# Kernel tuning notes

Measured on AMD Instinct MI355X. Metric: run time of the kernel, lower is better.

## Reference

```python
import jax, jax.numpy as jnp
import numpy as np

NUM_NODES = 40000
NUM_EDGES = 400000
DIM = 128
NUM_REL = 502  # num_relation * 2
NUM_HEAD = 1


def setup_inputs() -> dict:
    key = jax.random.key(0)
    ks = jax.random.split(key, 16)
    d = DIM
    return {
        "curr_stat": jax.random.normal(ks[0], (NUM_NODES, d), jnp.float32),
        "last_stat": jax.random.normal(ks[1], (NUM_NODES, d), jnp.float32),
        "relemb_weight": jax.random.normal(ks[2], (NUM_REL, d), jnp.float32),
        "selfrel_weight": jax.random.normal(ks[3], (1, d), jnp.float32),
        "Wq": jax.random.normal(ks[4], (2 * d, d), jnp.float32) * (1.0 / np.sqrt(2 * d)),
        "bq": jax.random.normal(ks[5], (d,), jnp.float32) * 0.02,
        "Wk": jax.random.normal(ks[6], (2 * d, d), jnp.float32) * (1.0 / np.sqrt(2 * d)),
        "bk": jax.random.normal(ks[7], (d,), jnp.float32) * 0.02,
        "Wv": jax.random.normal(ks[8], (d, d), jnp.float32) * (1.0 / np.sqrt(d)),
        "bv": jax.random.normal(ks[9], (d,), jnp.float32) * 0.02,
        "dyn_weight": jax.random.normal(ks[10], (d, d), jnp.float32) * (1.0 / np.sqrt(d)),
        "edge_index": jax.random.randint(ks[11], (2, NUM_EDGES), 0, NUM_NODES, jnp.int32),
        "edge_type": jax.random.randint(ks[12], (NUM_EDGES,), 0, NUM_REL, jnp.int32),
    }


def _segment_softmax(scores, seg, num_segments):
    # scores: [E, H]; softmax over edges sharing the same destination segment
    m = jax.ops.segment_max(scores, seg, num_segments=num_segments)  # [N, H]
    e = jnp.exp(scores - m[seg])
    s = jax.ops.segment_sum(e, seg, num_segments=num_segments)  # [N, H]
    return e / s[seg]


def reference(curr_stat, last_stat, relemb_weight, selfrel_weight,
              Wq, bq, Wk, bk, Wv, bv, dyn_weight,
              edge_index, edge_type):
    N, D = curr_stat.shape
    H = NUM_HEAD
    HD = D // H

    # append self-loop edges for every node, with the dedicated self-relation
    loop = jnp.arange(N, dtype=edge_index.dtype)
    src = jnp.concatenate([edge_index[0], loop])  # [E_total]
    dst = jnp.concatenate([edge_index[1], loop])  # [E_total]
    type_emb = jnp.concatenate(
        [relemb_weight[edge_type], jnp.broadcast_to(selfrel_weight, (N, D))], axis=0)

    E = src.shape[0]
    # linear projections (x @ W + b); torch Linear stores W transposed, same math
    q = (jnp.concatenate([curr_stat[dst], type_emb], -1) @ Wq + bq).reshape(E, H, HD)
    k = (jnp.concatenate([last_stat[src], type_emb], -1) @ Wk + bk).reshape(E, H, HD)
    v = (last_stat[src] @ Wv + bv).reshape(E, H, HD)

    attn = jnp.sum(q * k, axis=-1) / np.sqrt(HD).astype(np.float32)  # [E, H]

    dyn_prob = _segment_softmax(attn, dst, N)   # [E, H]
    sta_prob = _segment_softmax(-attn, dst, N)  # [E, H]

    counts = jax.ops.segment_sum(jnp.ones((E,), jnp.float32), dst, num_segments=N)
    denom = jnp.maximum(counts, 1.0)[:, None]  # scatter-mean denominator

    feat_dyn = jax.ops.segment_sum((dyn_prob[..., None] * v).reshape(E, D), dst,
                                   num_segments=N) / denom
    feat_sta = jax.ops.segment_sum((sta_prob[..., None] * v).reshape(E, D), dst,
                                   num_segments=N) / denom

    # stack (feat_sta, feat_dyn @ dyn_weight) -> [2, N, D]
    return jnp.stack([feat_sta, feat_dyn @ dyn_weight])
```

## Files before the change

kernel.cpp:

```cpp
#include <hip/hip_runtime.h>
#include <hip/hip_bf16.h>
#include <math.h>

#define DIMC 128

typedef __attribute__((ext_vector_type(8))) short short8;
typedef __attribute__((ext_vector_type(4))) float floatx4;

static __device__ __forceinline__ unsigned pk2(float lo, float hi) {
    __hip_bfloat162 h = __float22bfloat162_rn(make_float2(lo, hi));
    return *(unsigned*)&h;
}
static __device__ __forceinline__ unsigned short f2bf(float x) {
    union { float f; unsigned int u; } v; v.f = x;
    unsigned int r = v.u + 0x7FFFu + ((v.u >> 16) & 1u);
    return (unsigned short)(r >> 16);
}
static __device__ __forceinline__ float2 bf2f2(unsigned int u) {
    union { unsigned int i; float f; } a, b;
    a.i = u << 16; b.i = u & 0xFFFF0000u;
    return make_float2(a.f, b.f);
}

struct PrepArgs { const float* W[4]; unsigned short* F[4]; };

__global__ __launch_bounds__(64) void prep_wfrag(PrepArgs a)
{
    int mat = blockIdx.y;
    int ts  = blockIdx.x;
    int s = ts & 3, t = ts >> 2;
    int lane = threadIdx.x;
    int q = lane >> 4, c = lane & 15;
    const float* W = a.W[mat];
    unsigned short o[8];
    #pragma unroll
    for (int j = 0; j < 8; ++j)
        o[j] = f2bf(W[(long)(s * 32 + q * 8 + j) * DIMC + t * 16 + c]);
    uint4 u;
    u.x = (unsigned)o[0] | ((unsigned)o[1] << 16);
    u.y = (unsigned)o[2] | ((unsigned)o[3] << 16);
    u.z = (unsigned)o[4] | ((unsigned)o[5] << 16);
    u.w = (unsigned)o[6] | ((unsigned)o[7] << 16);
    ((uint4*)a.F[mat])[ts * 64 + lane] = u;
}

struct GemmM3 {
    const float*          Af[3];
    const unsigned short* Ab[3];
    const unsigned short* F[3];
    const float*          bias[3];
    float*                outf[3];
    unsigned short*       outb[3];
    int                   ostride[3];
    int                   ooff[3];
};

__global__ __launch_bounds__(256) void gemm_mfma(GemmM3 g, int M)
{
    const int which = blockIdx.y;
    const float*          __restrict__ Af   = g.Af[which];
    const unsigned short* __restrict__ Ab   = g.Ab[which];
    const unsigned short* __restrict__ F    = g.F[which];
    const float*          __restrict__ bias = g.bias[which];
    float*          __restrict__ outf = g.outf[which];
    unsigned short* __restrict__ outb = g.outb[which];
    const int ostride = g.ostride[which];
    const int ooff    = g.ooff[which];

    const int wave = threadIdx.x >> 6;
    const int lane = threadIdx.x & 63;
    const int q = lane >> 4, c = lane & 15;
    const int rowbase = blockIdx.x * 64 + wave * 16;

    short8 wf[8][4];
    const uint4* Fp = (const uint4*)F;
    #pragma unroll
    for (int t = 0; t < 8; ++t)
        #pragma unroll
        for (int s = 0; s < 4; ++s) {
            uint4 u = Fp[(t * 4 + s) * 64 + lane];
            wf[t][s] = *(short8*)&u;
        }

    floatx4 acc[8];
    #pragma unroll
    for (int t = 0; t < 8; ++t) {
        float b = bias ? bias[t * 16 + c] : 0.0f;
        acc[t] = (floatx4){b, b, b, b};
    }

    short8 af[4];
    if (Af) {
        const float* Ar = Af + (long)(rowbase + c) * DIMC + q * 8;
        #pragma unroll
        for (int s = 0; s < 4; ++s) {
            float4 x0 = *(const float4*)(Ar + s * 32);
            float4 x1 = *(const float4*)(Ar + s * 32 + 4);
            uint4 u;
            u.x = pk2(x0.x, x0.y);
            u.y = pk2(x0.z, x0.w);
            u.z = pk2(x1.x, x1.y);
            u.w = pk2(x1.z, x1.w);
            af[s] = *(short8*)&u;
        }
    } else {
        const unsigned short* Ar = Ab + (long)(rowbase + c) * DIMC + q * 8;
        #pragma unroll
        for (int s = 0; s < 4; ++s) {
            uint4 u = *(const uint4*)(Ar + s * 32);
            af[s] = *(short8*)&u;
        }
    }

    #pragma unroll
    for (int t = 0; t < 8; ++t)
        #pragma unroll
        for (int s = 0; s < 4; ++s)
            acc[t] = __builtin_amdgcn_mfma_f32_16x16x32_bf16(af[s], wf[t][s], acc[t], 0, 0, 0);

    if (outf) {
        #pragma unroll
        for (int t = 0; t < 8; ++t)
            #pragma unroll
            for (int r = 0; r < 4; ++r)
                outf[(long)(rowbase + q * 4 + r) * DIMC + t * 16 + c] = acc[t][r];
    } else {
        #pragma unroll
        for (int t = 0; t < 8; ++t)
            #pragma unroll
            for (int r = 0; r < 4; ++r) {
                float other = __shfl_xor(acc[t][r], 1);
                if ((lane & 1) == 0) {
                    unsigned word = pk2(acc[t][r], other);
                    ((unsigned*)outb)[((long)(rowbase + q * 4 + r) * 64 + t * 8 + (c >> 1))
                                      * (long)ostride + ooff] = word;
                }
            }
    }
}

__global__ __launch_bounds__(128) void rel_proj(
    const float* __restrict__ relemb, const float* __restrict__ selfrel,
    const float* __restrict__ Wq, const float* __restrict__ bq,
    const float* __restrict__ Wk, const float* __restrict__ bk,
    uint2* __restrict__ QKre, int R)
{
    int t = blockIdx.x;
    int c = threadIdx.x;
    const float* row = (t < R) ? (relemb + (long)t * DIMC) : selfrel;
    float aq = bq[c], ak = bk[c];
    for (int k = 0; k < DIMC; ++k) {
        float a = row[k];
        aq = fmaf(a, Wq[(long)(DIMC + k) * DIMC + c], aq);
        ak = fmaf(a, Wk[(long)(DIMC + k) * DIMC + c], ak);
    }
    float aqo = __shfl_xor(aq, 1);
    float ako = __shfl_xor(ak, 1);
    if ((c & 1) == 0)
        QKre[(long)t * 64 + (c >> 1)] = make_uint2(pk2(aq, aqo), pk2(ak, ako));
}

__global__ void zero_int(int* __restrict__ p, int n) {
    int i = blockIdx.x * blockDim.x + threadIdx.x;
    if (i < n) p[i] = 0;
}

__global__ void hist_kernel(const int* __restrict__ dst, int* __restrict__ deg, int E) {
    int e = blockIdx.x * blockDim.x + threadIdx.x;
    if (e < E) atomicAdd(&deg[dst[e]], 1);
}

__global__ __launch_bounds__(256) void partial_sums(const int* __restrict__ deg,
                                                    int* __restrict__ partial, int N)
{
    __shared__ int sh[256];
    int t = threadIdx.x;
    int beg = blockIdx.x * 1024 + t * 4;
    int s = 0;
    if (beg + 3 < N) { int4 v = *(const int4*)(deg + beg); s = v.x + v.y + v.z + v.w; }
    else { for (int j = 0; j < 4; ++j) if (beg + j < N) s += deg[beg + j]; }
    sh[t] = s;
    __syncthreads();
    for (int d = 128; d >= 1; d >>= 1) {
        if (t < d) sh[t] += sh[t + d];
        __syncthreads();
    }
    if (t == 0) partial[blockIdx.x] = sh[0];
}

__global__ __launch_bounds__(256) void scan_partials(int* __restrict__ partial, int nb)
{
    __shared__ int sh[256];
    int t = threadIdx.x;
    sh[t] = (t < nb) ? partial[t] : 0;
    __syncthreads();
    for (int d = 1; d < 256; d <<= 1) {
        int v = (t >= d) ? sh[t - d] : 0;
        __syncthreads();
        sh[t] += v;
        __syncthreads();
    }
    if (t < nb) partial[t] = (t == 0) ? 0 : sh[t - 1];
}

__global__ __launch_bounds__(256) void write_offsets(const int* __restrict__ deg,
                                                     const int* __restrict__ partial,
                                                     int* __restrict__ offs,
                                                     int* __restrict__ cursor, int N)
{
    __shared__ int sh[256];
    int t = threadIdx.x;
    int beg = blockIdx.x * 1024 + t * 4;
    int d0 = 0, d1 = 0, d2 = 0, d3 = 0;
    if (beg + 3 < N) { int4 v = *(const int4*)(deg + beg); d0 = v.x; d1 = v.y; d2 = v.z; d3 = v.w; }
    else {
        if (beg < N)     d0 = deg[beg];
        if (beg + 1 < N) d1 = deg[beg + 1];
        if (beg + 2 < N) d2 = deg[beg + 2];
        if (beg + 3 < N) d3 = deg[beg + 3];
    }
    int s = d0 + d1 + d2 + d3;
    sh[t] = s;
    __syncthreads();
    for (int d = 1; d < 256; d <<= 1) {
        int v = (t >= d) ? sh[t - d] : 0;
        __syncthreads();
        sh[t] += v;
        __syncthreads();
    }
    int base = partial[blockIdx.x] + sh[t] - s;
    int o0 = base, o1 = o0 + d0, o2 = o1 + d1, o3 = o2 + d2;
    if (beg < N)     { offs[beg]     = o0; cursor[beg]     = o0; }
    if (beg + 1 < N) { offs[beg + 1] = o1; cursor[beg + 1] = o1; }
    if (beg + 2 < N) { offs[beg + 2] = o2; cursor[beg + 2] = o2; }
    if (beg + 3 < N) { offs[beg + 3] = o3; cursor[beg + 3] = o3; }
}

__global__ void scatter_kernel(const int* __restrict__ src, const int* __restrict__ dst,
                               const int* __restrict__ etype, int* __restrict__ cursor,
                               int2* __restrict__ sedge, int E)
{
    int e = blockIdx.x * blockDim.x + threadIdx.x;
    if (e < E) {
        int d = dst[e];
        int p = atomicAdd(&cursor[d], 1);
        sedge[p] = make_int2(src[e], etype[e]);
    }
}

__global__ __launch_bounds__(256) void node_kernel(
    const float* __restrict__ Qn,
    const uint2* __restrict__ KV,
    const uint2* __restrict__ QKre,
    const int* __restrict__ offs, const int* __restrict__ deg,
    const int2* __restrict__ sedge,
    float* __restrict__ out_sta, unsigned* __restrict__ feat_dyn,
    int N, int R)
{
    int n = (blockIdx.x * blockDim.x + threadIdx.x) >> 6;
    int lane = threadIdx.x & 63;
    if (n >= N) return;

    const float cs = 0.08838834764831845f * 1.4426950408889634f;
    int base = offs[n];
    int dcnt = deg[n];

    float2 qn = ((const float2*)(Qn + (long)n * DIMC))[lane];

    uint2 kvs = KV[(unsigned)n * 64u + lane];
    uint2 qks = QKre[(unsigned)R * 64u + lane];
    float2 ks = bf2f2(kvs.x), vs = bf2f2(kvs.y);
    float2 qr = bf2f2(qks.x), kr = bf2f2(qks.y);
    float p = (qn.x + qr.x) * (ks.x + kr.x) + (qn.y + qr.y) * (ks.y + kr.y);
    #pragma unroll
    for (int m = 32; m >= 1; m >>= 1) p += __shfl_xor(p, m);
    float a_self = p * cs;

    float m_dyn = a_self, s_dyn = 1.0f;
    float m_sta = -a_self, s_sta = 1.0f;
    float2 accd = vs;
    float2 accs = vs;

    int i = 0;
    for (; i + 4 <= dcnt; i += 4) {
        int2 e0 = sedge[base + i],     e1 = sedge[base + i + 1];
        int2 e2 = sedge[base + i + 2], e3 = sedge[base + i + 3];

        uint2 kv0 = KV[(unsigned)e0.x * 64u + lane];
        uint2 kv1 = KV[(unsigned)e1.x * 64u + lane];
        uint2 kv2 = KV[(unsigned)e2.x * 64u + lane];
        uint2 kv3 = KV[(unsigned)e3.x * 64u + lane];
        uint2 t0 = QKre[(unsigned)e0.y * 64u + lane];
        uint2 t1 = QKre[(unsigned)e1.y * 64u + lane];
        uint2 t2 = QKre[(unsigned)e2.y * 64u + lane];
        uint2 t3 = QKre[(unsigned)e3.y * 64u + lane];

        float2 kn0 = bf2f2(kv0.x), v0 = bf2f2(kv0.y);
        float2 kn1 = bf2f2(kv1.x), v1 = bf2f2(kv1.y);
        float2 kn2 = bf2f2(kv2.x), v2 = bf2f2(kv2.y);
        float2 kn3 = bf2f2(kv3.x), v3 = bf2f2(kv3.y);
        float2 q0 = bf2f2(t0.x), k0 = bf2f2(t0.y);
        float2 q1 = bf2f2(t1.x), k1 = bf2f2(t1.y);
        float2 q2 = bf2f2(t2.x), k2 = bf2f2(t2.y);
        float2 q3 = bf2f2(t3.x), k3 = bf2f2(t3.y);

        float p0 = (qn.x + q0.x) * (kn0.x + k0.x) + (qn.y + q0.y) * (kn0.y + k0.y);
        float p1 = (qn.x + q1.x) * (kn1.x + k1.x) + (qn.y + q1.y) * (kn1.y + k1.y);
        float p2 = (qn.x + q2.x) * (kn2.x + k2.x) + (qn.y + q2.y) * (kn2.y + k2.y);
        float p3 = (qn.x + q3.x) * (kn3.x + k3.x) + (qn.y + q3.y) * (kn3.y + k3.y);
        #pragma unroll
        for (int m = 32; m >= 1; m >>= 1) {
            p0 += __shfl_xor(p0, m);
            p1 += __shfl_xor(p1, m);
            p2 += __shfl_xor(p2, m);
            p3 += __shfl_xor(p3, m);
        }
        float a0 = p0 * cs, a1 = p1 * cs, a2 = p2 * cs, a3 = p3 * cs;

        float mx = fmaxf(fmaxf(a0, a1), fmaxf(a2, a3));
        float mn = fmaxf(m_dyn, mx);
        float f  = exp2f(m_dyn - mn);
        float w0 = exp2f(a0 - mn), w1 = exp2f(a1 - mn);
        float w2 = exp2f(a2 - mn), w3 = exp2f(a3 - mn);
        s_dyn = fmaf(s_dyn, f, (w0 + w1) + (w2 + w3));
        accd.x = fmaf(accd.x, f, fmaf(w0, v0.x, fmaf(w1, v1.x, fmaf(w2, v2.x, w3 * v3.x))));
        accd.y = fmaf(accd.y, f, fmaf(w0, v0.y, fmaf(w1, v1.y, fmaf(w2, v2.y, w3 * v3.y))));
        m_dyn = mn;

        float nmx = -fminf(fminf(a0, a1), fminf(a2, a3));
        float ms = fmaxf(m_sta, nmx);
        float fs = exp2f(m_sta - ms);
        float u0 = exp2f(-a0 - ms), u1 = exp2f(-a1 - ms);
        float u2 = exp2f(-a2 - ms), u3 = exp2f(-a3 - ms);
        s_sta = fmaf(s_sta, fs, (u0 + u1) + (u2 + u3));
        accs.x = fmaf(accs.x, fs, fmaf(u0, v0.x, fmaf(u1, v1.x, fmaf(u2, v2.x, u3 * v3.x))));
        accs.y = fmaf(accs.y, fs, fmaf(u0, v0.y, fmaf(u1, v1.y, fmaf(u2, v2.y, u3 * v3.y))));
        m_sta = ms;
    }

    for (; i < dcnt; ++i) {
        int2 e = sedge[base + i];
        uint2 kv = KV[(unsigned)e.x * 64u + lane];
        uint2 tt = QKre[(unsigned)e.y * 64u + lane];
        float2 kn = bf2f2(kv.x), v = bf2f2(kv.y);
        float2 q2 = bf2f2(tt.x), k2 = bf2f2(tt.y);
        float pp = (qn.x + q2.x) * (kn.x + k2.x) + (qn.y + q2.y) * (kn.y + k2.y);
        #pragma unroll
        for (int m = 32; m >= 1; m >>= 1) pp += __shfl_xor(pp, m);
        float a = pp * cs;

        float mn = fmaxf(m_dyn, a);
        float fd = exp2f(m_dyn - mn);
        float wd = exp2f(a - mn);
        s_dyn = fmaf(s_dyn, fd, wd);
        accd.x = fmaf(accd.x, fd, wd * v.x);
        accd.y = fmaf(accd.y, fd, wd * v.y);
        m_dyn = mn;

        float ms = fmaxf(m_sta, -a);
        float fs = exp2f(m_sta - ms);
        float ws_ = exp2f(-a - ms);
        s_sta = fmaf(s_sta, fs, ws_);
        accs.x = fmaf(accs.x, fs, ws_ * v.x);
        accs.y = fmaf(accs.y, fs, ws_ * v.y);
        m_sta = ms;
    }

    float denom = (float)(dcnt + 1);
    float id_ = 1.0f / (s_dyn * denom);
    float is_ = 1.0f / (s_sta * denom);
    ((float2*)(out_sta + (long)n * DIMC))[lane] = make_float2(accs.x * is_, accs.y * is_);
    feat_dyn[(unsigned)n * 64u + lane] = pk2(accd.x * id_, accd.y * id_);
}

extern "C" void kernel_launch(void* const* d_in, const int* in_sizes, int n_in,
                              void* d_out, int out_size, void* d_ws, size_t ws_size,
                              hipStream_t stream)
{
    const float* curr    = (const float*)d_in[0];
    const float* last    = (const float*)d_in[1];
    const float* relemb  = (const float*)d_in[2];
    const float* selfrel = (const float*)d_in[3];
    const float* Wq      = (const float*)d_in[4];
    const float* bq      = (const float*)d_in[5];
    const float* Wk      = (const float*)d_in[6];
    const float* bk      = (const float*)d_in[7];
    const float* Wv      = (const float*)d_in[8];
    const float* bv      = (const float*)d_in[9];
    const float* dynw    = (const float*)d_in[10];
    const int*   eidx    = (const int*)d_in[11];
    const int*   etype   = (const int*)d_in[12];
    float* out = (float*)d_out;

    const int N = in_sizes[0] / DIMC;
    const int E = in_sizes[12];
    const int R = in_sizes[2] / DIMC;
    const int* esrc = eidx;
    const int* edst = eidx + E;

    char* wp = (char*)d_ws;
    auto alloc = [&](size_t bytes) { char* r = wp; wp += (bytes + 15) & ~(size_t)15; return r; };
    size_t nd = (size_t)N * DIMC;
    float*          Qn    = (float*)alloc(nd * 4);
    uint2*          KV    = (uint2*)alloc((size_t)N * 64 * 8);
    unsigned short* Fdb   = (unsigned short*)alloc(nd * 2);
    uint2*          QKre  = (uint2*)alloc((size_t)(R + 1) * 64 * 8);
    unsigned short* FWq   = (unsigned short*)alloc(2048 * 8 * 2);
    unsigned short* FWk   = (unsigned short*)alloc(2048 * 8 * 2);
    unsigned short* FWv   = (unsigned short*)alloc(2048 * 8 * 2);
    unsigned short* FWd   = (unsigned short*)alloc(2048 * 8 * 2);
    int*            deg   = (int*)alloc((size_t)N * 4);
    int*            offs  = (int*)alloc((size_t)N * 4);
    int*            cursor= (int*)alloc((size_t)N * 4);
    int2*           sedge = (int2*)alloc((size_t)E * 8);
    int*            partial = (int*)alloc(256 * 4);

    const int gblk = N / 64;
    const int sblk = (N + 1023) / 1024;

    PrepArgs pa;
    pa.W[0] = Wq;   pa.F[0] = FWq;
    pa.W[1] = Wk;   pa.F[1] = FWk;
    pa.W[2] = Wv;   pa.F[2] = FWv;
    pa.W[3] = dynw; pa.F[3] = FWd;
    hipLaunchKernelGGL(prep_wfrag, dim3(32, 4), dim3(64), 0, stream, pa);

    GemmM3 qkv;
    qkv.Af[0] = curr; qkv.Ab[0] = nullptr; qkv.F[0] = FWq; qkv.bias[0] = nullptr;
    qkv.outf[0] = Qn; qkv.outb[0] = nullptr; qkv.ostride[0] = 1; qkv.ooff[0] = 0;
    qkv.Af[1] = last; qkv.Ab[1] = nullptr; qkv.F[1] = FWk; qkv.bias[1] = nullptr;
    qkv.outf[1] = nullptr; qkv.outb[1] = (unsigned short*)KV; qkv.ostride[1] = 2; qkv.ooff[1] = 0;
    qkv.Af[2] = last; qkv.Ab[2] = nullptr; qkv.F[2] = FWv; qkv.bias[2] = bv;
    qkv.outf[2] = nullptr; qkv.outb[2] = (unsigned short*)KV; qkv.ostride[2] = 2; qkv.ooff[2] = 1;
    hipLaunchKernelGGL(gemm_mfma, dim3(gblk, 3), dim3(256), 0, stream, qkv, N);

    hipLaunchKernelGGL(rel_proj, dim3(R + 1), dim3(128), 0, stream,
                       relemb, selfrel, Wq, bq, Wk, bk, QKre, R);
    hipLaunchKernelGGL(zero_int, dim3((N + 255) / 256), dim3(256), 0, stream, deg, N);
    hipLaunchKernelGGL(hist_kernel, dim3((E + 255) / 256), dim3(256), 0, stream, edst, deg, E);
    hipLaunchKernelGGL(partial_sums, dim3(sblk), dim3(256), 0, stream, deg, partial, N);
    hipLaunchKernelGGL(scan_partials, dim3(1), dim3(256), 0, stream, partial, sblk);
    hipLaunchKernelGGL(write_offsets, dim3(sblk), dim3(256), 0, stream,
                       deg, partial, offs, cursor, N);
    hipLaunchKernelGGL(scatter_kernel, dim3((E + 255) / 256), dim3(256), 0, stream,
                       esrc, edst, etype, cursor, sedge, E);
    hipLaunchKernelGGL(node_kernel, dim3((N + 3) / 4), dim3(256), 0, stream,
                       Qn, KV, QKre, offs, deg, sedge, out, (unsigned*)Fdb, N, R);

    GemmM3 fin;
    fin.Af[0] = nullptr; fin.Ab[0] = Fdb; fin.F[0] = FWd; fin.bias[0] = nullptr;
    fin.outf[0] = out + nd; fin.outb[0] = nullptr; fin.ostride[0] = 1; fin.ooff[0] = 0;
    fin.Af[1] = nullptr; fin.Ab[1] = Fdb; fin.F[1] = FWd; fin.bias[1] = nullptr;
    fin.outf[1] = out + nd; fin.outb[1] = nullptr; fin.ostride[1] = 1; fin.ooff[1] = 0;
    fin.Af[2] = nullptr; fin.Ab[2] = Fdb; fin.F[2] = FWd; fin.bias[2] = nullptr;
    fin.outf[2] = out + nd; fin.outb[2] = nullptr; fin.ostride[2] = 1; fin.ooff[2] = 0;
    hipLaunchKernelGGL(gemm_mfma, dim3(gblk, 1), dim3(256), 0, stream, fin, N);
}
```

Baseline: 243.0 us.

## Split node edges across half-waves and merge prep, relation projection into MFMA GEMM

The node kernel now gives each destination node two 32-lane halves that each process alternate pairs of edges with 16-byte vector loads. The halves merge their online-softmax state with a cross-half shuffle at the end, which halves the shuffle-reduction depth per edge and widens the gathers. The scalar relation-projection kernel and the zero-fill kernel are removed. Relation embeddings are copied into a staging buffer and projected by the MFMA GEMM as two extra batched slices, and weight-fragment prep, the embedding copy and the degree zeroing share one launch. This cuts launch count and the slow FMA loop, at the cost of masked extra edge loads and added bounds checks in the GEMM.

```diff
diff --git a/kernel.cpp b/kernel.cpp
--- a/kernel.cpp
+++ b/kernel.cpp
@@ -22,42 +22,63 @@
     return make_float2(a.f, b.f);
 }
 
-struct PrepArgs { const float* W[4]; unsigned short* F[4]; };
-
-__global__ __launch_bounds__(64) void prep_wfrag(PrepArgs a)
-{
-    int mat = blockIdx.y;
-    int ts  = blockIdx.x;
-    int s = ts & 3, t = ts >> 2;
+struct PrepArgs {
+    const float* W[6];
+    unsigned short* F[6];
+    const float* relemb; const float* selfrel;
+    float* TypeEmb;
+    int* deg;
+    int R; int N;
+};
+
+__global__ __launch_bounds__(64) void prep_all(PrepArgs a)
+{
+    int b = blockIdx.x;
     int lane = threadIdx.x;
-    int q = lane >> 4, c = lane & 15;
-    const float* W = a.W[mat];
-    unsigned short o[8];
-    #pragma unroll
-    for (int j = 0; j < 8; ++j)
-        o[j] = f2bf(W[(long)(s * 32 + q * 8 + j) * DIMC + t * 16 + c]);
-    uint4 u;
-    u.x = (unsigned)o[0] | ((unsigned)o[1] << 16);
-    u.y = (unsigned)o[2] | ((unsigned)o[3] << 16);
-    u.z = (unsigned)o[4] | ((unsigned)o[5] << 16);
-    u.w = (unsigned)o[6] | ((unsigned)o[7] << 16);
-    ((uint4*)a.F[mat])[ts * 64 + lane] = u;
-}
-
-struct GemmM3 {
-    const float*          Af[3];
-    const unsigned short* Ab[3];
-    const unsigned short* F[3];
-    const float*          bias[3];
-    float*                outf[3];
-    unsigned short*       outb[3];
-    int                   ostride[3];
-    int                   ooff[3];
+    if (b < 192) {
+        int mat = b >> 5, ts = b & 31;
+        int s = ts & 3, t = ts >> 2;
+        int q = lane >> 4, c = lane & 15;
+        const float* W = a.W[mat];
+        unsigned short o[8];
+        #pragma unroll
+        for (int j = 0; j < 8; ++j)
+            o[j] = f2bf(W[(long)(s * 32 + q * 8 + j) * DIMC + t * 16 + c]);
+        uint4 u;
+        u.x = (unsigned)o[0] | ((unsigned)o[1] << 16);
+        u.y = (unsigned)o[2] | ((unsigned)o[3] << 16);
+        u.z = (unsigned)o[4] | ((unsigned)o[5] << 16);
+        u.w = (unsigned)o[6] | ((unsigned)o[7] << 16);
+        ((uint4*)a.F[mat])[ts * 64 + lane] = u;
+    } else if (b < 192 + a.R + 1) {
+        int r = b - 192;
+        const float* src = (r < a.R) ? (a.relemb + (long)r * DIMC) : a.selfrel;
+        float2 v = ((const float2*)src)[lane];
+        ((float2*)(a.TypeEmb + (long)r * DIMC))[lane] = v;
+    } else {
+        int i = (b - (192 + a.R + 1)) * 64 + lane;
+        if (i < a.N) a.deg[i] = 0;
+    }
+}
+
+struct GemmM5 {
+    const float*          Af[5];
+    const unsigned short* Ab[5];
+    const unsigned short* F[5];
+    const float*          bias[5];
+    float*                outf[5];
+    unsigned short*       outb[5];
+    int                   ostride[5];
+    int                   ooff[5];
+    int                   M[5];
 };
 
-__global__ __launch_bounds__(256) void gemm_mfma(GemmM3 g, int M)
+__global__ __launch_bounds__(256) void gemm_mfma(GemmM5 g)
 {
     const int which = blockIdx.y;
+    const int M = g.M[which];
+    if (blockIdx.x * 64 >= M) return;
+
     const float*          __restrict__ Af   = g.Af[which];
     const unsigned short* __restrict__ Ab   = g.Ab[which];
     const unsigned short* __restrict__ F    = g.F[which];
@@ -89,9 +110,10 @@
         acc[t] = (floatx4){b, b, b, b};
     }
 
+    int rowA = rowbase + c; if (rowA > M - 1) rowA = M - 1;
     short8 af[4];
     if (Af) {
-        const float* Ar = Af + (long)(rowbase + c) * DIMC + q * 8;
+        const float* Ar = Af + (long)rowA * DIMC + q * 8;
         #pragma unroll
         for (int s = 0; s < 4; ++s) {
             float4 x0 = *(const float4*)(Ar + s * 32);
@@ -104,7 +126,7 @@
             af[s] = *(short8*)&u;
         }
     } else {
-        const unsigned short* Ar = Ab + (long)(rowbase + c) * DIMC + q * 8;
+        const unsigned short* Ar = Ab + (long)rowA * DIMC + q * 8;
         #pragma unroll
         for (int s = 0; s < 4; ++s) {
             uint4 u = *(const uint4*)(Ar + s * 32);
@@ -122,47 +144,25 @@
         #pragma unroll
         for (int t = 0; t < 8; ++t)
             #pragma unroll
-            for (int r = 0; r < 4; ++r)
-                outf[(long)(rowbase + q * 4 + r) * DIMC + t * 16 + c] = acc[t][r];
+            for (int r = 0; r < 4; ++r) {
+                int row = rowbase + q * 4 + r;
+                if (row < M)
+                    outf[(long)row * DIMC + t * 16 + c] = acc[t][r];
+            }
     } else {
         #pragma unroll
         for (int t = 0; t < 8; ++t)
             #pragma unroll
             for (int r = 0; r < 4; ++r) {
                 float other = __shfl_xor(acc[t][r], 1);
-                if ((lane & 1) == 0) {
+                int row = rowbase + q * 4 + r;
+                if ((lane & 1) == 0 && row < M) {
                     unsigned word = pk2(acc[t][r], other);
-                    ((unsigned*)outb)[((long)(rowbase + q * 4 + r) * 64 + t * 8 + (c >> 1))
+                    ((unsigned*)outb)[((long)row * 64 + t * 8 + (c >> 1))
                                       * (long)ostride + ooff] = word;
                 }
             }
     }
-}
-
-__global__ __launch_bounds__(128) void rel_proj(
-    const float* __restrict__ relemb, const float* __restrict__ selfrel,
-    const float* __restrict__ Wq, const float* __restrict__ bq,
-    const float* __restrict__ Wk, const float* __restrict__ bk,
-    uint2* __restrict__ QKre, int R)
-{
-    int t = blockIdx.x;
-    int c = threadIdx.x;
-    const float* row = (t < R) ? (relemb + (long)t * DIMC) : selfrel;
-    float aq = bq[c], ak = bk[c];
-    for (int k = 0; k < DIMC; ++k) {
-        float a = row[k];
-        aq = fmaf(a, Wq[(long)(DIMC + k) * DIMC + c], aq);
-        ak = fmaf(a, Wk[(long)(DIMC + k) * DIMC + c], ak);
-    }
-    float aqo = __shfl_xor(aq, 1);
-    float ako = __shfl_xor(ak, 1);
-    if ((c & 1) == 0)
-        QKre[(long)t * 64 + (c >> 1)] = make_uint2(pk2(aq, aqo), pk2(ak, ako));
-}
-
-__global__ void zero_int(int* __restrict__ p, int n) {
-    int i = blockIdx.x * blockDim.x + threadIdx.x;
-    if (i < n) p[i] = 0;
 }
 
 __global__ void hist_kernel(const int* __restrict__ dst, int* __restrict__ deg, int E) {
@@ -250,127 +250,154 @@
 
 __global__ __launch_bounds__(256) void node_kernel(
     const float* __restrict__ Qn,
-    const uint2* __restrict__ KV,
-    const uint2* __restrict__ QKre,
+    const uint4* __restrict__ KV4,
+    const uint4* __restrict__ QK4,
     const int* __restrict__ offs, const int* __restrict__ deg,
     const int2* __restrict__ sedge,
-    float* __restrict__ out_sta, unsigned* __restrict__ feat_dyn,
+    float* __restrict__ out_sta, uint2* __restrict__ feat_dyn,
     int N, int R)
 {
     int n = (blockIdx.x * blockDim.x + threadIdx.x) >> 6;
     int lane = threadIdx.x & 63;
     if (n >= N) return;
+    const int hl = lane & 31;
+    const int h  = lane >> 5;
 
     const float cs = 0.08838834764831845f * 1.4426950408889634f;
     int base = offs[n];
     int dcnt = deg[n];
 
-    float2 qn = ((const float2*)(Qn + (long)n * DIMC))[lane];
-
-    uint2 kvs = KV[(unsigned)n * 64u + lane];
-    uint2 qks = QKre[(unsigned)R * 64u + lane];
-    float2 ks = bf2f2(kvs.x), vs = bf2f2(kvs.y);
-    float2 qr = bf2f2(qks.x), kr = bf2f2(qks.y);
-    float p = (qn.x + qr.x) * (ks.x + kr.x) + (qn.y + qr.y) * (ks.y + kr.y);
-    #pragma unroll
-    for (int m = 32; m >= 1; m >>= 1) p += __shfl_xor(p, m);
-    float a_self = p * cs;
-
-    float m_dyn = a_self, s_dyn = 1.0f;
-    float m_sta = -a_self, s_sta = 1.0f;
-    float2 accd = vs;
-    float2 accs = vs;
-
-    int i = 0;
-    for (; i + 4 <= dcnt; i += 4) {
-        int2 e0 = sedge[base + i],     e1 = sedge[base + i + 1];
-        int2 e2 = sedge[base + i + 2], e3 = sedge[base + i + 3];
-
-        uint2 kv0 = KV[(unsigned)e0.x * 64u + lane];
-        uint2 kv1 = KV[(unsigned)e1.x * 64u + lane];
-        uint2 kv2 = KV[(unsigned)e2.x * 64u + lane];
-        uint2 kv3 = KV[(unsigned)e3.x * 64u + lane];
-        uint2 t0 = QKre[(unsigned)e0.y * 64u + lane];
-        uint2 t1 = QKre[(unsigned)e1.y * 64u + lane];
-        uint2 t2 = QKre[(unsigned)e2.y * 64u + lane];
-        uint2 t3 = QKre[(unsigned)e3.y * 64u + lane];
-
-        float2 kn0 = bf2f2(kv0.x), v0 = bf2f2(kv0.y);
-        float2 kn1 = bf2f2(kv1.x), v1 = bf2f2(kv1.y);
-        float2 kn2 = bf2f2(kv2.x), v2 = bf2f2(kv2.y);
-        float2 kn3 = bf2f2(kv3.x), v3 = bf2f2(kv3.y);
-        float2 q0 = bf2f2(t0.x), k0 = bf2f2(t0.y);
-        float2 q1 = bf2f2(t1.x), k1 = bf2f2(t1.y);
-        float2 q2 = bf2f2(t2.x), k2 = bf2f2(t2.y);
-        float2 q3 = bf2f2(t3.x), k3 = bf2f2(t3.y);
-
-        float p0 = (qn.x + q0.x) * (kn0.x + k0.x) + (qn.y + q0.y) * (kn0.y + k0.y);
-        float p1 = (qn.x + q1.x) * (kn1.x + k1.x) + (qn.y + q1.y) * (kn1.y + k1.y);
-        float p2 = (qn.x + q2.x) * (kn2.x + k2.x) + (qn.y + q2.y) * (kn2.y + k2.y);
-        float p3 = (qn.x + q3.x) * (kn3.x + k3.x) + (qn.y + q3.y) * (kn3.y + k3.y);
-        #pragma unroll
-        for (int m = 32; m >= 1; m >>= 1) {
-            p0 += __shfl_xor(p0, m);
-            p1 += __shfl_xor(p1, m);
-            p2 += __shfl_xor(p2, m);
-            p3 += __shfl_xor(p3, m);
-        }
-        float a0 = p0 * cs, a1 = p1 * cs, a2 = p2 * cs, a3 = p3 * cs;
-
-        float mx = fmaxf(fmaxf(a0, a1), fmaxf(a2, a3));
-        float mn = fmaxf(m_dyn, mx);
-        float f  = exp2f(m_dyn - mn);
-        float w0 = exp2f(a0 - mn), w1 = exp2f(a1 - mn);
-        float w2 = exp2f(a2 - mn), w3 = exp2f(a3 - mn);
-        s_dyn = fmaf(s_dyn, f, (w0 + w1) + (w2 + w3));
-        accd.x = fmaf(accd.x, f, fmaf(w0, v0.x, fmaf(w1, v1.x, fmaf(w2, v2.x, w3 * v3.x))));
-        accd.y = fmaf(accd.y, f, fmaf(w0, v0.y, fmaf(w1, v1.y, fmaf(w2, v2.y, w3 * v3.y))));
-        m_dyn = mn;
-
-        float nmx = -fminf(fminf(a0, a1), fminf(a2, a3));
-        float ms = fmaxf(m_sta, nmx);
-        float fs = exp2f(m_sta - ms);
-        float u0 = exp2f(-a0 - ms), u1 = exp2f(-a1 - ms);
-        float u2 = exp2f(-a2 - ms), u3 = exp2f(-a3 - ms);
-        s_sta = fmaf(s_sta, fs, (u0 + u1) + (u2 + u3));
-        accs.x = fmaf(accs.x, fs, fmaf(u0, v0.x, fmaf(u1, v1.x, fmaf(u2, v2.x, u3 * v3.x))));
-        accs.y = fmaf(accs.y, fs, fmaf(u0, v0.y, fmaf(u1, v1.y, fmaf(u2, v2.y, u3 * v3.y))));
-        m_sta = ms;
-    }
-
-    for (; i < dcnt; ++i) {
-        int2 e = sedge[base + i];
-        uint2 kv = KV[(unsigned)e.x * 64u + lane];
-        uint2 tt = QKre[(unsigned)e.y * 64u + lane];
-        float2 kn = bf2f2(kv.x), v = bf2f2(kv.y);
-        float2 q2 = bf2f2(tt.x), k2 = bf2f2(tt.y);
-        float pp = (qn.x + q2.x) * (kn.x + k2.x) + (qn.y + q2.y) * (kn.y + k2.y);
-        #pragma unroll
-        for (int m = 32; m >= 1; m >>= 1) pp += __shfl_xor(pp, m);
-        float a = pp * cs;
-
-        float mn = fmaxf(m_dyn, a);
-        float fd = exp2f(m_dyn - mn);
-        float wd = exp2f(a - mn);
-        s_dyn = fmaf(s_dyn, fd, wd);
-        accd.x = fmaf(accd.x, fd, wd * v.x);
-        accd.y = fmaf(accd.y, fd, wd * v.y);
-        m_dyn = mn;
-
-        float ms = fmaxf(m_sta, -a);
-        float fs = exp2f(m_sta - ms);
-        float ws_ = exp2f(-a - ms);
-        s_sta = fmaf(s_sta, fs, ws_);
-        accs.x = fmaf(accs.x, fs, ws_ * v.x);
-        accs.y = fmaf(accs.y, fs, ws_ * v.y);
-        m_sta = ms;
-    }
-
-    float denom = (float)(dcnt + 1);
-    float id_ = 1.0f / (s_dyn * denom);
-    float is_ = 1.0f / (s_sta * denom);
-    ((float2*)(out_sta + (long)n * DIMC))[lane] = make_float2(accs.x * is_, accs.y * is_);
-    feat_dyn[(unsigned)n * 64u + lane] = pk2(accd.x * id_, accd.y * id_);
+    float4 qn = ((const float4*)(Qn + (long)n * DIMC))[hl];
+
+    uint4 kvs = KV4[(unsigned)n * 32u + hl];
+    uint4 qks = QK4[(unsigned)R * 32u + hl];
+    {
+        float2 k0 = bf2f2(kvs.x), k1 = bf2f2(kvs.z);
+        float2 qr0 = bf2f2(qks.x), qr1 = bf2f2(qks.z);
+        float2 kr0 = bf2f2(qks.y), kr1 = bf2f2(qks.w);
+        float p = (qn.x + qr0.x) * (k0.x + kr0.x)
+                + (qn.y + qr0.y) * (k0.y + kr0.y)
+                + (qn.z + qr1.x) * (k1.x + kr1.x)
+                + (qn.w + qr1.y) * (k1.y + kr1.y);
+        #pragma unroll
+        for (int m = 16; m >= 1; m >>= 1) p += __shfl_xor(p, m);
+        kvs.x = __float_as_uint(p);
+        qks.x = 0;
+        float a_self = p * cs;
+        float2 v0 = bf2f2(kvs.y), v1 = bf2f2(kvs.w);
+        float m_d, s_d, m_s, s_s; float4 accd, accs;
+        if (h == 0) {
+            m_d = a_self;  s_d = 1.0f;
+            m_s = -a_self; s_s = 1.0f;
+            accd = make_float4(v0.x, v0.y, v1.x, v1.y);
+            accs = accd;
+        } else {
+            m_d = -1e30f; s_d = 0.0f;
+            m_s = -1e30f; s_s = 0.0f;
+            accd = make_float4(0.f, 0.f, 0.f, 0.f);
+            accs = accd;
+        }
+
+        int T = (dcnt + 3) >> 2;
+        for (int it = 0; it < T; ++it) {
+            int iA = 4 * it + 2 * h, iB = iA + 1;
+            bool vA = iA < dcnt, vB = iB < dcnt;
+            int2 eA = sedge[vA ? (base + iA) : 0];
+            int2 eB = sedge[vB ? (base + iB) : 0];
+            uint4 kvA = KV4[(unsigned)eA.x * 32u + hl];
+            uint4 kvB = KV4[(unsigned)eB.x * 32u + hl];
+            uint4 qkA = QK4[(unsigned)eA.y * 32u + hl];
+            uint4 qkB = QK4[(unsigned)eB.y * 32u + hl];
+
+            float2 ka0 = bf2f2(kvA.x), ka1 = bf2f2(kvA.z);
+            float2 qa0 = bf2f2(qkA.x), qa1 = bf2f2(qkA.z);
+            float2 ra0 = bf2f2(qkA.y), ra1 = bf2f2(qkA.w);
+            float pA = (qn.x + qa0.x) * (ka0.x + ra0.x)
+                     + (qn.y + qa0.y) * (ka0.y + ra0.y)
+                     + (qn.z + qa1.x) * (ka1.x + ra1.x)
+                     + (qn.w + qa1.y) * (ka1.y + ra1.y);
+            float2 kb0 = bf2f2(kvB.x), kb1 = bf2f2(kvB.z);
+            float2 qb0 = bf2f2(qkB.x), qb1 = bf2f2(qkB.z);
+            float2 rb0 = bf2f2(qkB.y), rb1 = bf2f2(qkB.w);
+            float pB = (qn.x + qb0.x) * (kb0.x + rb0.x)
+                     + (qn.y + qb0.y) * (kb0.y + rb0.y)
+                     + (qn.z + qb1.x) * (kb1.x + rb1.x)
+                     + (qn.w + qb1.y) * (kb1.y + rb1.y);
+            #pragma unroll
+            for (int m = 16; m >= 1; m >>= 1) {
+                pA += __shfl_xor(pA, m);
+                pB += __shfl_xor(pB, m);
+            }
+            float aA = pA * cs, aB = pB * cs;
+            float dA = vA ? aA : -1e30f, dB = vB ? aB : -1e30f;
+            float nA = vA ? -aA : -1e30f, nB = vB ? -aB : -1e30f;
+
+            float2 va0 = bf2f2(kvA.y), va1 = bf2f2(kvA.w);
+            float2 vb0 = bf2f2(kvB.y), vb1 = bf2f2(kvB.w);
+
+            {
+                float mn = fmaxf(m_d, fmaxf(dA, dB));
+                float f  = exp2f(m_d - mn);
+                float wA = vA ? exp2f(dA - mn) : 0.0f;
+                float wB = vB ? exp2f(dB - mn) : 0.0f;
+                s_d = fmaf(s_d, f, wA + wB);
+                accd.x = fmaf(accd.x, f, fmaf(wA, va0.x, wB * vb0.x));
+                accd.y = fmaf(accd.y, f, fmaf(wA, va0.y, wB * vb0.y));
+                accd.z = fmaf(accd.z, f, fmaf(wA, va1.x, wB * vb1.x));
+                accd.w = fmaf(accd.w, f, fmaf(wA, va1.y, wB * vb1.y));
+                m_d = mn;
+            }
+            {
+                float mn = fmaxf(m_s, fmaxf(nA, nB));
+                float f  = exp2f(m_s - mn);
+                float wA = vA ? exp2f(nA - mn) : 0.0f;
+                float wB = vB ? exp2f(nB - mn) : 0.0f;
+                s_s = fmaf(s_s, f, wA + wB);
+                accs.x = fmaf(accs.x, f, fmaf(wA, va0.x, wB * vb0.x));
+                accs.y = fmaf(accs.y, f, fmaf(wA, va0.y, wB * vb0.y));
+                accs.z = fmaf(accs.z, f, fmaf(wA, va1.x, wB * vb1.x));
+                accs.w = fmaf(accs.w, f, fmaf(wA, va1.y, wB * vb1.y));
+                m_s = mn;
+            }
+        }
+
+        {
+            float mo = __shfl_xor(m_d, 32), so = __shfl_xor(s_d, 32);
+            float4 ao;
+            ao.x = __shfl_xor(accd.x, 32); ao.y = __shfl_xor(accd.y, 32);
+            ao.z = __shfl_xor(accd.z, 32); ao.w = __shfl_xor(accd.w, 32);
+            float M = fmaxf(m_d, mo);
+            float f0 = exp2f(m_d - M), f1 = exp2f(mo - M);
+            s_d = fmaf(s_d, f0, so * f1);
+            accd.x = fmaf(accd.x, f0, ao.x * f1);
+            accd.y = fmaf(accd.y, f0, ao.y * f1);
+            accd.z = fmaf(accd.z, f0, ao.z * f1);
+            accd.w = fmaf(accd.w, f0, ao.w * f1);
+        }
+        {
+            float mo = __shfl_xor(m_s, 32), so = __shfl_xor(s_s, 32);
+            float4 ao;
+            ao.x = __shfl_xor(accs.x, 32); ao.y = __shfl_xor(accs.y, 32);
+            ao.z = __shfl_xor(accs.z, 32); ao.w = __shfl_xor(accs.w, 32);
+            float M = fmaxf(m_s, mo);
+            float f0 = exp2f(m_s - M), f1 = exp2f(mo - M);
+            s_s = fmaf(s_s, f0, so * f1);
+            accs.x = fmaf(accs.x, f0, ao.x * f1);
+            accs.y = fmaf(accs.y, f0, ao.y * f1);
+            accs.z = fmaf(accs.z, f0, ao.z * f1);
+            accs.w = fmaf(accs.w, f0, ao.w * f1);
+        }
+
+        if (h == 0) {
+            float denom = (float)(dcnt + 1);
+            float id_ = 1.0f / (s_d * denom);
+            float is_ = 1.0f / (s_s * denom);
+            ((float4*)(out_sta + (long)n * DIMC))[hl] =
+                make_float4(accs.x * is_, accs.y * is_, accs.z * is_, accs.w * is_);
+            feat_dyn[(unsigned)n * 32u + hl] =
+                make_uint2(pk2(accd.x * id_, accd.y * id_), pk2(accd.z * id_, accd.w * id_));
+        }
+    }
 }
 
 extern "C" void kernel_launch(void* const* d_in, const int* in_sizes, int n_in,
@@ -402,13 +429,12 @@
     auto alloc = [&](size_t bytes) { char* r = wp; wp += (bytes + 15) & ~(size_t)15; return r; };
     size_t nd = (size_t)N * DIMC;
     float*          Qn    = (float*)alloc(nd * 4);
-    uint2*          KV    = (uint2*)alloc((size_t)N * 64 * 8);
+    uint4*          KV    = (uint4*)alloc((size_t)N * 32 * 16);
     unsigned short* Fdb   = (unsigned short*)alloc(nd * 2);
-    uint2*          QKre  = (uint2*)alloc((size_t)(R + 1) * 64 * 8);
-    unsigned short* FWq   = (unsigned short*)alloc(2048 * 8 * 2);
-    unsigned short* FWk   = (unsigned short*)alloc(2048 * 8 * 2);
-    unsigned short* FWv   = (unsigned short*)alloc(2048 * 8 * 2);
-    unsigned short* FWd   = (unsigned short*)alloc(2048 * 8 * 2);
+    uint4*          QKre  = (uint4*)alloc((size_t)(R + 1) * 32 * 16);
+    float*          TypeEmb = (float*)alloc((size_t)(R + 2) * DIMC * 4);
+    unsigned short* FW[6];
+    for (int m = 0; m < 6; ++m) FW[m] = (unsigned short*)alloc(2048 * 8 * 2);
     int*            deg   = (int*)alloc((size_t)N * 4);
     int*            offs  = (int*)alloc((size_t)N * 4);
     int*            cursor= (int*)alloc((size_t)N * 4);
@@ -419,24 +445,14 @@
     const int sblk = (N + 1023) / 1024;
 
     PrepArgs pa;
-    pa.W[0] = Wq;   pa.F[0] = FWq;
-    pa.W[1] = Wk;   pa.F[1] = FWk;
-    pa.W[2] = Wv;   pa.F[2] = FWv;
-    pa.W[3] = dynw; pa.F[3] = FWd;
-    hipLaunchKernelGGL(prep_wfrag, dim3(32, 4), dim3(64), 0, stream, pa);
-
-    GemmM3 qkv;
-    qkv.Af[0] = curr; qkv.Ab[0] = nullptr; qkv.F[0] = FWq; qkv.bias[0] = nullptr;
-    qkv.outf[0] = Qn; qkv.outb[0] = nullptr; qkv.ostride[0] = 1; qkv.ooff[0] = 0;
-    qkv.Af[1] = last; qkv.Ab[1] = nullptr; qkv.F[1] = FWk; qkv.bias[1] = nullptr;
-    qkv.outf[1] = nullptr; qkv.outb[1] = (unsigned short*)KV; qkv.ostride[1] = 2; qkv.ooff[1] = 0;
-    qkv.Af[2] = last; qkv.Ab[2] = nullptr; qkv.F[2] = FWv; qkv.bias[2] = bv;
-    qkv.outf[2] = nullptr; qkv.outb[2] = (unsigned short*)KV; qkv.ostride[2] = 2; qkv.ooff[2] = 1;
-    hipLaunchKernelGGL(gemm_mfma, dim3(gblk, 3), dim3(256), 0, stream, qkv, N);
-
-    hipLaunchKernelGGL(rel_proj, dim3(R + 1), dim3(128), 0, stream,
-                       relemb, selfrel, Wq, bq, Wk, bk, QKre, R);
-    hipLaunchKernelGGL(zero_int, dim3((N + 255) / 256), dim3(256), 0, stream, deg, N);
+    pa.W[0] = Wq;   pa.W[1] = Wk;   pa.W[2] = Wv;
+    pa.W[3] = dynw; pa.W[4] = Wq + (size_t)DIMC * DIMC; pa.W[5] = Wk + (size_t)DIMC * DIMC;
+    for (int m = 0; m < 6; ++m) pa.F[m] = FW[m];
+    pa.relemb = relemb; pa.selfrel = selfrel; pa.TypeEmb = TypeEmb;
+    pa.deg = deg; pa.R = R; pa.N = N;
+    int pgrid = 192 + (R + 1) + (N + 63) / 64;
+    hipLaunchKernelGGL(prep_all, dim3(pgrid), dim3(64), 0, stream, pa);
+
     hipLaunchKernelGGL(hist_kernel, dim3((E + 255) / 256), dim3(256), 0, stream, edst, deg, E);
     hipLaunchKernelGGL(partial_sums, dim3(sblk), dim3(256), 0, stream, deg, partial, N);
     hipLaunchKernelGGL(scan_partials, dim3(1), dim3(256), 0, stream, partial, sblk);
@@ -444,15 +460,27 @@
                        deg, partial, offs, cursor, N);
     hipLaunchKernelGGL(scatter_kernel, dim3((E + 255) / 256), dim3(256), 0, stream,
                        esrc, edst, etype, cursor, sedge, E);
+
+    GemmM5 g5;
+    for (int s = 0; s < 5; ++s) { g5.Ab[s] = nullptr; g5.outf[s] = nullptr; g5.outb[s] = nullptr; }
+    g5.Af[0] = curr;    g5.F[0] = FW[0]; g5.bias[0] = nullptr; g5.outf[0] = Qn;
+    g5.ostride[0] = 1;  g5.ooff[0] = 0;  g5.M[0] = N;
+    g5.Af[1] = last;    g5.F[1] = FW[1]; g5.bias[1] = nullptr; g5.outb[1] = (unsigned short*)KV;
+    g5.ostride[1] = 2;  g5.ooff[1] = 0;  g5.M[1] = N;
+    g5.Af[2] = last;    g5.F[2] = FW[2]; g5.bias[2] = bv;      g5.outb[2] = (unsigned short*)KV;
+    g5.ostride[2] = 2;  g5.ooff[2] = 1;  g5.M[2] = N;
+    g5.Af[3] = TypeEmb; g5.F[3] = FW[4]; g5.bias[3] = bq;      g5.outb[3] = (unsigned short*)QKre;
+    g5.ostride[3] = 2;  g5.ooff[3] = 0;  g5.M[3] = R + 1;
+    g5.Af[4] = TypeEmb; g5.F[4] = FW[5]; g5.bias[4] = bk;      g5.outb[4] = (unsigned short*)QKre;
+    g5.ostride[4] = 2;  g5.ooff[4] = 1;  g5.M[4] = R + 1;
+    hipLaunchKernelGGL(gemm_mfma, dim3(gblk, 5), dim3(256), 0, stream, g5);
+
     hipLaunchKernelGGL(node_kernel, dim3((N + 3) / 4), dim3(256), 0, stream,
-                       Qn, KV, QKre, offs, deg, sedge, out, (unsigned*)Fdb, N, R);
-
-    GemmM3 fin;
-    fin.Af[0] = nullptr; fin.Ab[0] = Fdb; fin.F[0] = FWd; fin.bias[0] = nullptr;
-    fin.outf[0] = out + nd; fin.outb[0] = nullptr; fin.ostride[0] = 1; fin.ooff[0] = 0;
-    fin.Af[1] = nullptr; fin.Ab[1] = Fdb; fin.F[1] = FWd; fin.bias[1] = nullptr;
-    fin.outf[1] = out + nd; fin.outb[1] = nullptr; fin.ostride[1] = 1; fin.ooff[1] = 0;
-    fin.Af[2] = nullptr; fin.Ab[2] = Fdb; fin.F[2] = FWd; fin.bias[2] = nullptr;
-    fin.outf[2] = out + nd; fin.outb[2] = nullptr; fin.ostride[2] = 1; fin.ooff[2] = 0;
-    hipLaunchKernelGGL(gemm_mfma, dim3(gblk, 1), dim3(256), 0, stream, fin, N);
-}
+                       Qn, KV, QKre, offs, deg, sedge, out, (uint2*)Fdb, N, R);
+
+    GemmM5 gf;
+    for (int s = 0; s < 5; ++s) { gf.Af[s] = nullptr; gf.Ab[s] = nullptr; gf.outf[s] = nullptr; gf.outb[s] = nullptr; gf.M[s] = 0; }
+    gf.Ab[0] = Fdb; gf.F[0] = FW[3]; gf.bias[0] = nullptr; gf.outf[0] = out + nd;
+    gf.ostride[0] = 1; gf.ooff[0] = 0; gf.M[0] = N;
+    hipLaunchKernelGGL(gemm_mfma, dim3(gblk, 1), dim3(256), 0, stream, gf);
+}
```

Result: no change. 242.1 us (-0.4%).
